# Kernel tuning notes

Hardware: AMD Instinct MI355X
Metric: run time of the kernel (lower is better)

## Reference

```python
import math
import jax, jax.numpy as jnp
import numpy as np

B, N, D = 16, 2048, 128
MASK_VALUE = -1000000.0


def setup_inputs() -> dict:
    key = jax.random.key(0)
    k1, k2, k3, k4 = jax.random.split(key, 4)
    queries = jax.random.normal(k1, (B, N, D), dtype=jnp.float32)
    keys = jax.random.normal(k2, (B, N, D), dtype=jnp.float32)
    values = jax.random.normal(k3, (B, N, D), dtype=jnp.float32)
    valid_lens = jax.random.randint(k4, (B,), 0, N, dtype=jnp.int32)
    return {"queries": queries, "keys": keys, "values": values, "valid_lens": valid_lens}


def reference(queries, keys, values, valid_lens):
    d = queries.shape[-1]
    # [B, Nq, Nk] full score matrix, as in the original bmm
    scores = jnp.einsum("bqd,bkd->bqk", queries, keys) / math.sqrt(d)
    # Faithful to the source bug: valid_lens.dim (a method) != 1, so it is
    # flattened and scores[idx][valid_len:] = -1e6 masks QUERY ROWS >= valid_len.
    row_idx = jnp.arange(scores.shape[1])  # [Nq]
    row_mask = row_idx[None, :, None] >= valid_lens[:, None, None]  # [B, Nq, 1]
    scores = jnp.where(row_mask, MASK_VALUE, scores)
    attn = jax.nn.softmax(scores, axis=-1)
    # dropout p=0.0 -> identity
    return jnp.einsum("bqk,bkd->bqd", attn, values)
```

## Files before the change

kernel.cpp:

```cpp
#include <hip/hip_runtime.h>

#define BN 2048
#define DD 128

typedef __attribute__((ext_vector_type(8))) short bf8;
typedef __attribute__((ext_vector_type(16))) float f16v;

__device__ __forceinline__ short bf16rne(float f) {
    unsigned u = __float_as_uint(f);
    u = (u + 0x7FFFu + ((u >> 16) & 1u)) >> 16;
    return (short)u;
}

__launch_bounds__(256, 2)
__global__ void attn_kernel(const float* __restrict__ Q,
                            const float* __restrict__ K,
                            const float* __restrict__ V,
                            const int* __restrict__ VL,
                            float* __restrict__ O) {
    __shared__ short sK[128 * 128];
    __shared__ short sV[128 * 128];
    __shared__ short sP[4 * 32 * 64];

    const int tid  = threadIdx.x;
    const int wave = tid >> 6;
    const int lane = tid & 63;
    const int lw   = lane & 31;
    const int lh   = lane >> 5;
    const int rt   = wave & 1;
    const int kh   = wave >> 1;

    const int L  = blockIdx.x;
    const int b  = (L & 7) | (((L >> 3) & 1) << 3);
    const int qt = L >> 4;
    const int q0 = qt * 64;

    const int vlen = VL[b];

    constexpr float SCL2 = 1.4426950408889634f * 0.08838834764831845f;

    float sclm[16];
    #pragma unroll
    for (int reg = 0; reg < 16; ++reg) {
        int row = (reg & 3) + 8 * (reg >> 2) + 4 * lh;
        int qg = q0 + rt * 32 + row;
        sclm[reg] = (qg >= vlen) ? 0.0f : SCL2;
    }

    const size_t qoff = ((size_t)b * BN + q0 + rt * 32 + lw) * DD;
    bf8 qfrag[8];
    #pragma unroll
    for (int ks = 0; ks < 8; ++ks) {
        int d0 = ks * 16 + lh * 8;
        float4 f0 = *(const float4*)(Q + qoff + d0);
        float4 f1 = *(const float4*)(Q + qoff + d0 + 4);
        bf8 w;
        w[0] = bf16rne(f0.x); w[1] = bf16rne(f0.y);
        w[2] = bf16rne(f0.z); w[3] = bf16rne(f0.w);
        w[4] = bf16rne(f1.x); w[5] = bf16rne(f1.y);
        w[6] = bf16rne(f1.z); w[7] = bf16rne(f1.w);
        qfrag[ks] = w;
    }

    f16v oacc[4] = {};
    float l[16];
    #pragma unroll
    for (int i = 0; i < 16; ++i) l[i] = 0.0f;

    const int pbase = wave * (32 * 64);

    for (int it = 0; it < 16; ++it) {
        const int kb = it * 128;

        {
            int g  = tid & 15;
            int r0 = tid >> 4;
            #pragma unroll
            for (int i = 0; i < 8; ++i) {
                int r = r0 + 16 * i;
                const float* src = K + ((size_t)b * BN + kb + r) * DD + g * 8;
                float4 f0 = *(const float4*)(src);
                float4 f1 = *(const float4*)(src + 4);
                bf8 w;
                w[0] = bf16rne(f0.x); w[1] = bf16rne(f0.y);
                w[2] = bf16rne(f0.z); w[3] = bf16rne(f0.w);
                w[4] = bf16rne(f1.x); w[5] = bf16rne(f1.y);
                w[6] = bf16rne(f1.z); w[7] = bf16rne(f1.w);
                int sg = (g & 8) | ((g ^ r) & 7);
                *(bf8*)&sK[r * 128 + sg * 8] = w;
            }
        }
        {
            int dq  = tid & 31;
            int kg0 = tid >> 5;
            #pragma unroll
            for (int i = 0; i < 2; ++i) {
                int kg = kg0 + 8 * i;
                float vr[32];
                #pragma unroll
                for (int j = 0; j < 8; ++j) {
                    float4 t = *(const float4*)(V + ((size_t)b * BN + kb + kg * 8 + j) * DD + dq * 4);
                    vr[j * 4 + 0] = t.x; vr[j * 4 + 1] = t.y;
                    vr[j * 4 + 2] = t.z; vr[j * 4 + 3] = t.w;
                }
                #pragma unroll
                for (int c = 0; c < 4; ++c) {
                    int d = dq * 4 + c;
                    bf8 w;
                    #pragma unroll
                    for (int j = 0; j < 8; ++j) w[j] = bf16rne(vr[j * 4 + c]);
                    int sg = (kg & 8) | ((kg ^ d) & 7);
                    *(bf8*)&sV[d * 128 + sg * 8] = w;
                }
            }
        }
        __syncthreads();

        f16v s0 = {}, s1 = {};
        #pragma unroll
        for (int ks = 0; ks < 8; ++ks) {
            int g  = ks * 2 + lh;
            int r0 = kh * 64 + lw;
            int sgA = (g & 8) | ((g ^ r0) & 7);
            bf8 b0 = *(const bf8*)&sK[r0 * 128 + sgA * 8];
            s0 = __builtin_amdgcn_mfma_f32_32x32x16_bf16(qfrag[ks], b0, s0, 0, 0, 0);
            int r1 = r0 + 32;
            int sgB = (g & 8) | ((g ^ r1) & 7);
            bf8 b1 = *(const bf8*)&sK[r1 * 128 + sgB * 8];
            s1 = __builtin_amdgcn_mfma_f32_32x32x16_bf16(qfrag[ks], b1, s1, 0, 0, 0);
        }

        #pragma unroll
        for (int reg = 0; reg < 16; ++reg) {
            float p0 = __builtin_amdgcn_exp2f(s0[reg] * sclm[reg]);
            float p1 = __builtin_amdgcn_exp2f(s1[reg] * sclm[reg]);
            l[reg] += p0 + p1;
            int row = (reg & 3) + 8 * (reg >> 2) + 4 * lh;
            int g0 = lw >> 3;
            sP[pbase + row * 64 + ((g0 ^ row) & 7) * 8 + (lw & 7)] = bf16rne(p0);
            int g1 = 4 + (lw >> 3);
            sP[pbase + row * 64 + ((g1 ^ row) & 7) * 8 + (lw & 7)] = bf16rne(p1);
        }

        #pragma unroll
        for (int ks = 0; ks < 4; ++ks) {
            int gk  = ks * 2 + lh;
            int sgp = (gk ^ lw) & 7;
            bf8 pa = *(const bf8*)&sP[pbase + lw * 64 + sgp * 8];
            #pragma unroll
            for (int ot = 0; ot < 4; ++ot) {
                int d   = ot * 32 + lw;
                int gv  = kh * 8 + ks * 2 + lh;
                int sgv = (gv & 8) | ((gv ^ d) & 7);
                bf8 vb = *(const bf8*)&sV[d * 128 + sgv * 8];
                oacc[ot] = __builtin_amdgcn_mfma_f32_32x32x16_bf16(pa, vb, oacc[ot], 0, 0, 0);
            }
        }
        __syncthreads();
    }

    float* oSh = (float*)sK;
    float* lSh = (float*)sV;
    if (kh == 1) {
        #pragma unroll
        for (int ot = 0; ot < 4; ++ot) {
            #pragma unroll
            for (int reg = 0; reg < 16; ++reg) {
                int row = (reg & 3) + 8 * (reg >> 2) + 4 * lh;
                oSh[rt * 4096 + row * 128 + ot * 32 + lw] = oacc[ot][reg];
            }
        }
        #pragma unroll
        for (int reg = 0; reg < 16; ++reg)
            lSh[rt * 1024 + reg * 64 + lane] = l[reg];
    }
    __syncthreads();
    if (kh == 0) {
        #pragma unroll
        for (int reg = 0; reg < 16; ++reg)
            l[reg] += lSh[rt * 1024 + reg * 64 + lane];
        #pragma unroll
        for (int reg = 0; reg < 16; ++reg) {
            float t = l[reg];
            t += __shfl_xor(t, 1, 64);
            t += __shfl_xor(t, 2, 64);
            t += __shfl_xor(t, 4, 64);
            t += __shfl_xor(t, 8, 64);
            t += __shfl_xor(t, 16, 64);
            l[reg] = t;
        }
        #pragma unroll
        for (int ot = 0; ot < 4; ++ot) {
            #pragma unroll
            for (int reg = 0; reg < 16; ++reg) {
                int row = (reg & 3) + 8 * (reg >> 2) + 4 * lh;
                float val = oacc[ot][reg] + oSh[rt * 4096 + row * 128 + ot * 32 + lw];
                val /= l[reg];
                O[((size_t)b * BN + q0 + rt * 32 + row) * DD + ot * 32 + lw] = val;
            }
        }
    }
}

extern "C" void kernel_launch(void* const* d_in, const int* in_sizes, int n_in,
                              void* d_out, int out_size, void* d_ws, size_t ws_size,
                              hipStream_t stream) {
    const float* Q  = (const float*)d_in[0];
    const float* K  = (const float*)d_in[1];
    const float* V  = (const float*)d_in[2];
    const int*   VL = (const int*)d_in[3];
    float* O = (float*)d_out;
    attn_kernel<<<512, 256, 0, stream>>>(Q, K, V, VL, O);
}
```

Measured before the change: 185.1 us.

## Pre-convert K/V to swizzled bf16 and stream tiles via async LDS DMA

Adds a prep kernel that converts K and V to bf16 once per batch tile, storing them in the swizzled LDS layout in workspace (V transposed). The attention kernel then copies ready-made tiles into shared memory with global_load_lds and overlaps the next K/V loads with compute. This removes the repeated fp32 loads and conversions done by every query block. In exchange it adds a second launch plus workspace traffic, and the DMA/barrier ordering has to be exactly right. The old kernel is kept as a fallback when the workspace is too small.

After: 148.2 us. -20.0%, faster.

```diff
diff --git a/kernel.cpp b/kernel.cpp
--- a/kernel.cpp
+++ b/kernel.cpp
@@ -12,15 +12,85 @@
     return (short)u;
 }
 
+__device__ __forceinline__ bf8 cvt8(float4 f0, float4 f1) {
+    bf8 w;
+    w[0] = bf16rne(f0.x); w[1] = bf16rne(f0.y);
+    w[2] = bf16rne(f0.z); w[3] = bf16rne(f0.w);
+    w[4] = bf16rne(f1.x); w[5] = bf16rne(f1.y);
+    w[6] = bf16rne(f1.z); w[7] = bf16rne(f1.w);
+    return w;
+}
+
+__device__ __forceinline__ void dma16(const void* gsrc, void* ldst) {
+    __builtin_amdgcn_global_load_lds(
+        (const __attribute__((address_space(1))) void*)gsrc,
+        (__attribute__((address_space(3))) void*)ldst,
+        16, 0, 0);
+}
+
+__device__ __forceinline__ void dma_tile(short* lds, const short* g, int wave, int lane) {
+    const char* gp = (const char*)g + wave * 8192 + lane * 16;
+    char* lp = (char*)lds + wave * 8192 + lane * 16;
+    #pragma unroll
+    for (int c = 0; c < 8; ++c)
+        dma16(gp + c * 1024, lp + c * 1024);
+}
+
+__launch_bounds__(256, 4)
+__global__ void prep_kernel(const float* __restrict__ K, const float* __restrict__ V,
+                            short* __restrict__ KS, short* __restrict__ VS) {
+    __shared__ short tile[128 * 136];
+    const int t = threadIdx.x;
+    const int blk = blockIdx.x;
+    if (blk < 256) {
+        const int b = blk >> 4, it = blk & 15;
+        const float* src = K + ((size_t)b * BN + it * 128) * DD;
+        short* dst = KS + (((size_t)b * 16 + it) << 14);
+        #pragma unroll
+        for (int i = 0; i < 8; ++i) {
+            int gid = t + 256 * i;
+            int r = gid >> 4, g = gid & 15;
+            float4 f0 = *(const float4*)(src + r * DD + g * 8);
+            float4 f1 = *(const float4*)(src + r * DD + g * 8 + 4);
+            int sg = (g & 8) | ((g ^ r) & 7);
+            *(bf8*)&dst[r * 128 + sg * 8] = cvt8(f0, f1);
+        }
+    } else {
+        const int bb = blk - 256;
+        const int b = bb >> 4, it = bb & 15;
+        const float* src = V + ((size_t)b * BN + it * 128) * DD;
+        short* dst = VS + (((size_t)b * 16 + it) << 14);
+        #pragma unroll
+        for (int i = 0; i < 8; ++i) {
+            int gid = t + 256 * i;
+            int r = gid >> 4, g = gid & 15;
+            float4 f0 = *(const float4*)(src + r * DD + g * 8);
+            float4 f1 = *(const float4*)(src + r * DD + g * 8 + 4);
+            *(bf8*)&tile[r * 136 + g * 8] = cvt8(f0, f1);
+        }
+        __syncthreads();
+        #pragma unroll
+        for (int i = 0; i < 8; ++i) {
+            int gid = t + 256 * i;
+            int d = gid & 127, kg = gid >> 7;
+            bf8 w;
+            #pragma unroll
+            for (int j = 0; j < 8; ++j) w[j] = tile[(kg * 8 + j) * 136 + d];
+            int sg = (kg & 8) | ((kg ^ d) & 7);
+            *(bf8*)&dst[d * 128 + sg * 8] = w;
+        }
+    }
+}
+
 __launch_bounds__(256, 2)
-__global__ void attn_kernel(const float* __restrict__ Q,
-                            const float* __restrict__ K,
-                            const float* __restrict__ V,
-                            const int* __restrict__ VL,
-                            float* __restrict__ O) {
-    __shared__ short sK[128 * 128];
-    __shared__ short sV[128 * 128];
-    __shared__ short sP[4 * 32 * 64];
+__global__ void attn2(const float* __restrict__ Q,
+                      const short* __restrict__ KS,
+                      const short* __restrict__ VS,
+                      const int* __restrict__ VL,
+                      float* __restrict__ O) {
+    __shared__ short sK[16384];
+    __shared__ short sV[16384];
+    __shared__ short sP[8192];
 
     const int tid  = threadIdx.x;
     const int wave = tid >> 6;
@@ -36,16 +106,19 @@
     const int q0 = qt * 64;
 
     const int vlen = VL[b];
-
     constexpr float SCL2 = 1.4426950408889634f * 0.08838834764831845f;
 
     float sclm[16];
     #pragma unroll
     for (int reg = 0; reg < 16; ++reg) {
         int row = (reg & 3) + 8 * (reg >> 2) + 4 * lh;
-        int qg = q0 + rt * 32 + row;
-        sclm[reg] = (qg >= vlen) ? 0.0f : SCL2;
-    }
+        sclm[reg] = (q0 + rt * 32 + row >= vlen) ? 0.0f : SCL2;
+    }
+
+    const short* kbase = KS + (((size_t)b * 16) << 14);
+    const short* vbase = VS + (((size_t)b * 16) << 14);
+
+    dma_tile(sK, kbase, wave, lane);
 
     const size_t qoff = ((size_t)b * BN + q0 + rt * 32 + lw) * DD;
     bf8 qfrag[8];
@@ -54,12 +127,7 @@
         int d0 = ks * 16 + lh * 8;
         float4 f0 = *(const float4*)(Q + qoff + d0);
         float4 f1 = *(const float4*)(Q + qoff + d0 + 4);
-        bf8 w;
-        w[0] = bf16rne(f0.x); w[1] = bf16rne(f0.y);
-        w[2] = bf16rne(f0.z); w[3] = bf16rne(f0.w);
-        w[4] = bf16rne(f1.x); w[5] = bf16rne(f1.y);
-        w[6] = bf16rne(f1.z); w[7] = bf16rne(f1.w);
-        qfrag[ks] = w;
+        qfrag[ks] = cvt8(f0, f1);
     }
 
     f16v oacc[4] = {};
@@ -67,11 +135,153 @@
     #pragma unroll
     for (int i = 0; i < 16; ++i) l[i] = 0.0f;
 
-    const int pbase = wave * (32 * 64);
+    const int pbase = wave * 2048;
+
+    for (int it = 0; it < 16; ++it) {
+        __syncthreads();
+        dma_tile(sV, vbase + ((size_t)it << 14), wave, lane);
+
+        f16v s0 = {}, s1 = {};
+        #pragma unroll
+        for (int ks = 0; ks < 8; ++ks) {
+            int g  = ks * 2 + lh;
+            int r0 = kh * 64 + lw;
+            int sgA = (g & 8) | ((g ^ r0) & 7);
+            bf8 b0 = *(const bf8*)&sK[r0 * 128 + sgA * 8];
+            s0 = __builtin_amdgcn_mfma_f32_32x32x16_bf16(qfrag[ks], b0, s0, 0, 0, 0);
+            int r1 = r0 + 32;
+            int sgB = (g & 8) | ((g ^ r1) & 7);
+            bf8 b1 = *(const bf8*)&sK[r1 * 128 + sgB * 8];
+            s1 = __builtin_amdgcn_mfma_f32_32x32x16_bf16(qfrag[ks], b1, s1, 0, 0, 0);
+        }
+
+        #pragma unroll
+        for (int reg = 0; reg < 16; ++reg) {
+            float p0 = __builtin_amdgcn_exp2f(s0[reg] * sclm[reg]);
+            float p1 = __builtin_amdgcn_exp2f(s1[reg] * sclm[reg]);
+            l[reg] += p0 + p1;
+            int row = (reg & 3) + 8 * (reg >> 2) + 4 * lh;
+            int g0 = lw >> 3;
+            sP[pbase + row * 64 + ((g0 ^ row) & 7) * 8 + (lw & 7)] = bf16rne(p0);
+            int g1 = 4 + (lw >> 3);
+            sP[pbase + row * 64 + ((g1 ^ row) & 7) * 8 + (lw & 7)] = bf16rne(p1);
+        }
+
+        __syncthreads();
+        if (it < 15)
+            dma_tile(sK, kbase + ((size_t)(it + 1) << 14), wave, lane);
+
+        #pragma unroll
+        for (int ks = 0; ks < 4; ++ks) {
+            int gk  = ks * 2 + lh;
+            int sgp = (gk ^ lw) & 7;
+            bf8 pa = *(const bf8*)&sP[pbase + lw * 64 + sgp * 8];
+            #pragma unroll
+            for (int ot = 0; ot < 4; ++ot) {
+                int d   = ot * 32 + lw;
+                int gv  = kh * 8 + ks * 2 + lh;
+                int sgv = (gv & 8) | ((gv ^ d) & 7);
+                bf8 vb = *(const bf8*)&sV[d * 128 + sgv * 8];
+                oacc[ot] = __builtin_amdgcn_mfma_f32_32x32x16_bf16(pa, vb, oacc[ot], 0, 0, 0);
+            }
+        }
+    }
+
+    __syncthreads();
+
+    float* oSh = (float*)sK;
+    float* lSh = (float*)sV;
+    if (kh == 1) {
+        #pragma unroll
+        for (int ot = 0; ot < 4; ++ot) {
+            #pragma unroll
+            for (int reg = 0; reg < 16; ++reg) {
+                int row = (reg & 3) + 8 * (reg >> 2) + 4 * lh;
+                oSh[rt * 4096 + row * 128 + ot * 32 + lw] = oacc[ot][reg];
+            }
+        }
+        #pragma unroll
+        for (int reg = 0; reg < 16; ++reg)
+            lSh[rt * 1024 + reg * 64 + lane] = l[reg];
+    }
+    __syncthreads();
+    if (kh == 0) {
+        #pragma unroll
+        for (int reg = 0; reg < 16; ++reg)
+            l[reg] += lSh[rt * 1024 + reg * 64 + lane];
+        #pragma unroll
+        for (int reg = 0; reg < 16; ++reg) {
+            float t = l[reg];
+            t += __shfl_xor(t, 1, 64);
+            t += __shfl_xor(t, 2, 64);
+            t += __shfl_xor(t, 4, 64);
+            t += __shfl_xor(t, 8, 64);
+            t += __shfl_xor(t, 16, 64);
+            l[reg] = t;
+        }
+        #pragma unroll
+        for (int ot = 0; ot < 4; ++ot) {
+            #pragma unroll
+            for (int reg = 0; reg < 16; ++reg) {
+                int row = (reg & 3) + 8 * (reg >> 2) + 4 * lh;
+                float val = oacc[ot][reg] + oSh[rt * 4096 + row * 128 + ot * 32 + lw];
+                val /= l[reg];
+                O[((size_t)b * BN + q0 + rt * 32 + row) * DD + ot * 32 + lw] = val;
+            }
+        }
+    }
+}
+
+__launch_bounds__(256, 2)
+__global__ void attn_v1(const float* __restrict__ Q,
+                        const float* __restrict__ K,
+                        const float* __restrict__ V,
+                        const int* __restrict__ VL,
+                        float* __restrict__ O) {
+    __shared__ short sK[128 * 128];
+    __shared__ short sV[128 * 128];
+    __shared__ short sP[4 * 32 * 64];
+
+    const int tid  = threadIdx.x;
+    const int wave = tid >> 6;
+    const int lane = tid & 63;
+    const int lw   = lane & 31;
+    const int lh   = lane >> 5;
+    const int rt   = wave & 1;
+    const int kh   = wave >> 1;
+
+    const int L  = blockIdx.x;
+    const int b  = (L & 7) | (((L >> 3) & 1) << 3);
+    const int qt = L >> 4;
+    const int q0 = qt * 64;
+    const int vlen = VL[b];
+    constexpr float SCL2 = 1.4426950408889634f * 0.08838834764831845f;
+
+    float sclm[16];
+    #pragma unroll
+    for (int reg = 0; reg < 16; ++reg) {
+        int row = (reg & 3) + 8 * (reg >> 2) + 4 * lh;
+        sclm[reg] = (q0 + rt * 32 + row >= vlen) ? 0.0f : SCL2;
+    }
+
+    const size_t qoff = ((size_t)b * BN + q0 + rt * 32 + lw) * DD;
+    bf8 qfrag[8];
+    #pragma unroll
+    for (int ks = 0; ks < 8; ++ks) {
+        int d0 = ks * 16 + lh * 8;
+        float4 f0 = *(const float4*)(Q + qoff + d0);
+        float4 f1 = *(const float4*)(Q + qoff + d0 + 4);
+        qfrag[ks] = cvt8(f0, f1);
+    }
+
+    f16v oacc[4] = {};
+    float l[16];
+    #pragma unroll
+    for (int i = 0; i < 16; ++i) l[i] = 0.0f;
+    const int pbase = wave * 2048;
 
     for (int it = 0; it < 16; ++it) {
         const int kb = it * 128;
-
         {
             int g  = tid & 15;
             int r0 = tid >> 4;
@@ -81,13 +291,8 @@
                 const float* src = K + ((size_t)b * BN + kb + r) * DD + g * 8;
                 float4 f0 = *(const float4*)(src);
                 float4 f1 = *(const float4*)(src + 4);
-                bf8 w;
-                w[0] = bf16rne(f0.x); w[1] = bf16rne(f0.y);
-                w[2] = bf16rne(f0.z); w[3] = bf16rne(f0.w);
-                w[4] = bf16rne(f1.x); w[5] = bf16rne(f1.y);
-                w[6] = bf16rne(f1.z); w[7] = bf16rne(f1.w);
                 int sg = (g & 8) | ((g ^ r) & 7);
-                *(bf8*)&sK[r * 128 + sg * 8] = w;
+                *(bf8*)&sK[r * 128 + sg * 8] = cvt8(f0, f1);
             }
         }
         {
@@ -210,5 +415,14 @@
     const float* V  = (const float*)d_in[2];
     const int*   VL = (const int*)d_in[3];
     float* O = (float*)d_out;
-    attn_kernel<<<512, 256, 0, stream>>>(Q, K, V, VL, O);
-}
+
+    const size_t need = (size_t)2 * 16 * 16 * 16384 * sizeof(short);
+    if (ws_size >= need) {
+        short* KS = (short*)d_ws;
+        short* VS = KS + (size_t)16 * 16 * 16384;
+        prep_kernel<<<512, 256, 0, stream>>>(K, V, KS, VS);
+        attn2<<<512, 256, 0, stream>>>(Q, KS, VS, VL, O);
+    } else {
+        attn_v1<<<512, 256, 0, stream>>>(Q, K, V, VL, O);
+    }
+}
```
